# Performance work log

Hardware: AMD Instinct MI355X
Metric: run time of the kernel (lower is better)

Reference implementation:

```python
import jax, jax.numpy as jnp
import numpy as np

# Model dims (match init_kwargs)
D_MODEL = 2048
N_HEADS = 16
N_GROUPS = 8
HEAD_DIM = 128
TPA_RANK = 2
TPA_Q_RANK = 6


def setup_inputs() -> dict:
    key = jax.random.key(0)
    ks = jax.random.split(key, 7)
    S, B = 4096, 2
    scale = 1.0 / np.sqrt(D_MODEL)
    inp = {
        "hidden_states": jax.random.normal(ks[0], (S, B, D_MODEL), jnp.float32),
        # weights stored [in, out] so projection is x @ W
        "W_a_q": jax.random.normal(ks[1], (D_MODEL, N_HEADS * TPA_Q_RANK), jnp.float32) * scale,
        "W_a_k": jax.random.normal(ks[2], (D_MODEL, N_GROUPS * TPA_RANK), jnp.float32) * scale,
        "W_a_v": jax.random.normal(ks[3], (D_MODEL, N_GROUPS * TPA_RANK), jnp.float32) * scale,
        "W_b_q": jax.random.normal(ks[4], (D_MODEL, TPA_Q_RANK * HEAD_DIM), jnp.float32) * scale,
        "W_b_k": jax.random.normal(ks[5], (D_MODEL, TPA_RANK * HEAD_DIM), jnp.float32) * scale,
        "W_b_v": jax.random.normal(ks[6], (D_MODEL, TPA_RANK * HEAD_DIM), jnp.float32) * scale,
    }
    return inp


def reference(hidden_states, W_a_q, W_a_k, W_a_v, W_b_q, W_b_k, W_b_v):
    S, B, _ = hidden_states.shape
    x = hidden_states
    # Six column-parallel projections (world_size=1 -> full outputs)
    a_q = (x @ W_a_q).reshape(S, B, N_HEADS, TPA_Q_RANK)
    a_k = (x @ W_a_k).reshape(S, B, N_GROUPS, TPA_RANK)
    a_v = (x @ W_a_v).reshape(S, B, N_GROUPS, TPA_RANK)
    b_q = (x @ W_b_q).reshape(S, B, TPA_Q_RANK, HEAD_DIM)
    b_k = (x @ W_b_k).reshape(S, B, TPA_RANK, HEAD_DIM)
    b_v = (x @ W_b_v).reshape(S, B, TPA_RANK, HEAD_DIM)
    # Low-rank reconstruction: per-token batched matmul over the tiny rank dim
    q = jnp.einsum('sbhr,sbrd->sbhd', a_q, b_q) / TPA_Q_RANK  # [S,B,H,D]
    k = jnp.einsum('sbgr,sbrd->sbgd', a_k, b_k) / TPA_RANK    # [S,B,G,D]
    v = jnp.einsum('sbgr,sbrd->sbgd', a_v, b_v) / TPA_RANK    # [S,B,G,D]
    heads_per_group = N_HEADS // N_GROUPS
    q = q.reshape(S, B, N_GROUPS, heads_per_group * HEAD_DIM)
    mixed_qkv = jnp.concatenate([q, k, v], axis=3).reshape(S, B, -1)
    return mixed_qkv
```

## Files before the change

kernel.cpp:

```cpp
#include <hip/hip_runtime.h>
#include <hip/hip_bf16.h>

typedef __bf16 bf16x8 __attribute__((ext_vector_type(8)));
typedef float  f32x4  __attribute__((ext_vector_type(4)));

#define GLOAD_LDS16(g, l) \
  __builtin_amdgcn_global_load_lds((const __attribute__((address_space(1))) void*)(g), \
                                   (__attribute__((address_space(3))) void*)(l), 16, 0, 0)

static __device__ __forceinline__ ushort f2bf(float f) {
  union { float f; unsigned u; } x; x.f = f;
  unsigned r = x.u + 0x7fffu + ((x.u >> 16) & 1u);
  return (ushort)(r >> 16);
}
static __device__ __forceinline__ float bf2f(ushort u) {
  union { unsigned u; float f; } x; x.u = ((unsigned)u) << 16;
  return x.f;
}

__global__ void cast_x_k(const float4* __restrict__ in, ushort4* __restrict__ out, int n4) {
  int idx = blockIdx.x * 256 + threadIdx.x;
  int stride = gridDim.x * 256;
  for (int i = idx; i < n4; i += stride) {
    float4 v = in[i];
    ushort4 o;
    o.x = f2bf(v.x); o.y = f2bf(v.y); o.z = f2bf(v.z); o.w = f2bf(v.w);
    out[i] = o;
  }
}

__global__ void pack_wt_k(const float* __restrict__ W0, const float* __restrict__ W1,
                          const float* __restrict__ W2, const float* __restrict__ W3,
                          const float* __restrict__ W4, const float* __restrict__ W5,
                          ushort* __restrict__ Wt) {
  __shared__ ushort tile[64 * 66];
  const int k0 = blockIdx.x * 64, c0 = blockIdx.y * 64;
  const int tid = threadIdx.x;
#pragma unroll
  for (int i = 0; i < 16; ++i) {
    int idx = tid + i * 256;
    int kl = idx >> 6, cl = idx & 63;
    int c = c0 + cl, k = k0 + kl;
    const float* W; int n, lc;
    if (c < 96)       { W = W0; n = 96;  lc = c; }
    else if (c < 112) { W = W1; n = 16;  lc = c - 96; }
    else if (c < 128) { W = W2; n = 16;  lc = c - 112; }
    else if (c < 896) { W = W3; n = 768; lc = c - 128; }
    else if (c < 1152){ W = W4; n = 256; lc = c - 896; }
    else              { W = W5; n = 256; lc = c - 1152; }
    tile[cl * 66 + kl] = f2bf(W[(size_t)k * n + lc]);
  }
  __syncthreads();
#pragma unroll
  for (int i = 0; i < 16; ++i) {
    int idx = tid + i * 256;
    int cl = idx >> 6, kl = idx & 63;
    Wt[(size_t)(c0 + cl) * 2048 + (k0 + kl)] = tile[cl * 66 + kl];
  }
}

__global__ __launch_bounds__(256) void gemm_bt_k(const ushort* __restrict__ X,
                                                 const ushort* __restrict__ Wt,
                                                 ushort* __restrict__ Y) {
  __shared__ ushort lds[2][8192];
  const int tid = threadIdx.x;
  const int w = tid >> 6, lane = tid & 63;
  const int bid = blockIdx.x;
  const int wg = (bid & 7) * 88 + (bid >> 3);
  const int bm = wg & 63, bn = wg >> 6;
  const int wr = w >> 1, wc = w & 1;

  const int s0 = w, s1 = w + 4;
  const int ra = s0 * 16 + (lane >> 2);
  const int rb = s1 * 16 + (lane >> 2);
  const int ga = (lane & 3) ^ ((ra >> 1) & 3);
  const int gb = (lane & 3) ^ ((rb >> 1) & 3);
  const ushort* gA0 = X  + (size_t)(bm * 128 + ra) * 2048 + ga * 8;
  const ushort* gA1 = X  + (size_t)(bm * 128 + rb) * 2048 + gb * 8;
  const ushort* gB0 = Wt + (size_t)(bn * 128 + ra) * 2048 + ga * 8;
  const ushort* gB1 = Wt + (size_t)(bn * 128 + rb) * 2048 + gb * 8;
  const int lo0 = s0 * 512, lo1 = s1 * 512;

  int offA[4], offB[4];
#pragma unroll
  for (int m = 0; m < 4; ++m) {
    int R = wr * 64 + m * 16 + (lane & 15);
    offA[m] = R * 32 + ((((lane >> 4) ^ ((R >> 1) & 3))) << 3);
    int C = wc * 64 + m * 16 + (lane & 15);
    offB[m] = 4096 + C * 32 + ((((lane >> 4) ^ ((C >> 1) & 3))) << 3);
  }

  GLOAD_LDS16(gA0, &lds[0][lo0]);
  GLOAD_LDS16(gA1, &lds[0][lo1]);
  GLOAD_LDS16(gB0, &lds[0][4096 + lo0]);
  GLOAD_LDS16(gB1, &lds[0][4096 + lo1]);
  __syncthreads();

  f32x4 acc[4][4] = {};
  int cur = 0;

  for (int kk = 0; kk < 64; ++kk) {
    if (kk < 63) {
      const int ko = (kk + 1) * 32;
      ushort* nb = lds[cur ^ 1];
      GLOAD_LDS16(gA0 + ko, nb + lo0);
      GLOAD_LDS16(gA1 + ko, nb + lo1);
      GLOAD_LDS16(gB0 + ko, nb + 4096 + lo0);
      GLOAD_LDS16(gB1 + ko, nb + 4096 + lo1);
    }
    const ushort* cb = lds[cur];
    bf16x8 a[4], b[4];
#pragma unroll
    for (int m = 0; m < 4; ++m) a[m] = *reinterpret_cast<const bf16x8*>(&cb[offA[m]]);
#pragma unroll
    for (int n = 0; n < 4; ++n) b[n] = *reinterpret_cast<const bf16x8*>(&cb[offB[n]]);
#pragma unroll
    for (int m = 0; m < 4; ++m)
#pragma unroll
      for (int n = 0; n < 4; ++n)
        acc[m][n] = __builtin_amdgcn_mfma_f32_16x16x32_bf16(a[m], b[n], acc[m][n], 0, 0, 0);

    __syncthreads();
    cur ^= 1;
  }

#pragma unroll
  for (int m = 0; m < 4; ++m) {
    int row0 = bm * 128 + wr * 64 + m * 16 + ((lane >> 4) << 2);
#pragma unroll
    for (int n = 0; n < 4; ++n) {
      int col = bn * 128 + wc * 64 + n * 16 + (lane & 15);
#pragma unroll
      for (int j = 0; j < 4; ++j)
        Y[(size_t)(row0 + j) * 1408 + col] = f2bf(acc[m][n][j]);
    }
  }
}

__global__ void recon_k(const ushort* __restrict__ Y, float4* __restrict__ out) {
  __shared__ float L[1408];
  const int t = blockIdx.x, tid = threadIdx.x;
  const ushort* src = Y + (size_t)t * 1408;
  if (tid < 176) {
    ushort4 v0 = ((const ushort4*)src)[tid * 2];
    ushort4 v1 = ((const ushort4*)src)[tid * 2 + 1];
    float* d = L + tid * 8;
    d[0] = bf2f(v0.x); d[1] = bf2f(v0.y); d[2] = bf2f(v0.z); d[3] = bf2f(v0.w);
    d[4] = bf2f(v1.x); d[5] = bf2f(v1.y); d[6] = bf2f(v1.z); d[7] = bf2f(v1.w);
  }
  __syncthreads();
  float4* o = out + (size_t)t * 1024;
#pragma unroll
  for (int i = 0; i < 4; ++i) {
    int q4 = tid + (i << 8);
    int p = q4 << 2;
    int g = p >> 9, sub = p & 511;
    float4 val;
    if (sub < 256) {
      int h = (g << 1) + (sub >> 7), d = sub & 127;
      const float* a = L + h * 6;
      const float* b = L + 128 + d;
#pragma unroll
      for (int c = 0; c < 4; ++c)
        (&val.x)[c] = (a[0] * b[c] + a[1] * b[128 + c] + a[2] * b[256 + c] +
                       a[3] * b[384 + c] + a[4] * b[512 + c] + a[5] * b[640 + c]) * (1.0f / 6.0f);
    } else if (sub < 384) {
      int d = sub - 256;
      float a0 = L[96 + (g << 1)], a1 = L[97 + (g << 1)];
#pragma unroll
      for (int c = 0; c < 4; ++c)
        (&val.x)[c] = 0.5f * (a0 * L[896 + d + c] + a1 * L[1024 + d + c]);
    } else {
      int d = sub - 384;
      float a0 = L[112 + (g << 1)], a1 = L[113 + (g << 1)];
#pragma unroll
      for (int c = 0; c < 4; ++c)
        (&val.x)[c] = 0.5f * (a0 * L[1152 + d + c] + a1 * L[1280 + d + c]);
    }
    o[q4] = val;
  }
}

extern "C" void kernel_launch(void* const* d_in, const int* in_sizes, int n_in,
                              void* d_out, int out_size, void* d_ws, size_t ws_size,
                              hipStream_t stream) {
  const float* x   = (const float*)d_in[0];
  const float* Waq = (const float*)d_in[1];
  const float* Wak = (const float*)d_in[2];
  const float* Wav = (const float*)d_in[3];
  const float* Wbq = (const float*)d_in[4];
  const float* Wbk = (const float*)d_in[5];
  const float* Wbv = (const float*)d_in[6];

  ushort* Xbf = (ushort*)d_ws;
  ushort* Wt  = (ushort*)((char*)d_ws + 33554432);
  ushort* Y   = (ushort*)((char*)d_ws + 39321600);
  float*  out = (float*)d_out;

  cast_x_k<<<2048, 256, 0, stream>>>((const float4*)x, (ushort4*)Xbf, 16777216 / 4);
  pack_wt_k<<<dim3(32, 22), 256, 0, stream>>>(Waq, Wak, Wav, Wbq, Wbk, Wbv, Wt);
  gemm_bt_k<<<704, 256, 0, stream>>>(Xbf, Wt, Y);
  recon_k<<<8192, 256, 0, stream>>>(Y, (float4*)out);
}
```

Before: 274.2 us.

## Triple-buffer GEMM LDS with explicit vmcnt waits and barriers

The GEMM main loop goes from double buffering to a three-stage LDS ring. Each stage is prefetched two steps ahead, and a partial s_waitcnt vmcnt lets the loop wait only for the oldest stage instead of doing a full __syncthreads drain. This is meant to hide global-to-LDS load latency behind MFMA work. LDS use grows from 32KB to 48KB per block, which may lower occupancy. The hand-written waitcnt and barrier sequence is fragile if the compiler emits other memory ops.

```diff
diff --git a/kernel.cpp b/kernel.cpp
--- a/kernel.cpp
+++ b/kernel.cpp
@@ -62,7 +62,7 @@
 __global__ __launch_bounds__(256) void gemm_bt_k(const ushort* __restrict__ X,
                                                  const ushort* __restrict__ Wt,
                                                  ushort* __restrict__ Y) {
-  __shared__ ushort lds[2][8192];
+  __shared__ ushort lds[3 * 8192];
   const int tid = threadIdx.x;
   const int w = tid >> 6, lane = tid & 63;
   const int bid = blockIdx.x;
@@ -90,39 +90,70 @@
     offB[m] = 4096 + C * 32 + ((((lane >> 4) ^ ((C >> 1) & 3))) << 3);
   }
 
-  GLOAD_LDS16(gA0, &lds[0][lo0]);
-  GLOAD_LDS16(gA1, &lds[0][lo1]);
-  GLOAD_LDS16(gB0, &lds[0][4096 + lo0]);
-  GLOAD_LDS16(gB1, &lds[0][4096 + lo1]);
-  __syncthreads();
-
   f32x4 acc[4][4] = {};
-  int cur = 0;
-
-  for (int kk = 0; kk < 64; ++kk) {
-    if (kk < 63) {
-      const int ko = (kk + 1) * 32;
-      ushort* nb = lds[cur ^ 1];
-      GLOAD_LDS16(gA0 + ko, nb + lo0);
-      GLOAD_LDS16(gA1 + ko, nb + lo1);
-      GLOAD_LDS16(gB0 + ko, nb + 4096 + lo0);
-      GLOAD_LDS16(gB1 + ko, nb + 4096 + lo1);
-    }
-    const ushort* cb = lds[cur];
-    bf16x8 a[4], b[4];
-#pragma unroll
-    for (int m = 0; m < 4; ++m) a[m] = *reinterpret_cast<const bf16x8*>(&cb[offA[m]]);
-#pragma unroll
-    for (int n = 0; n < 4; ++n) b[n] = *reinterpret_cast<const bf16x8*>(&cb[offB[n]]);
-#pragma unroll
-    for (int m = 0; m < 4; ++m)
-#pragma unroll
-      for (int n = 0; n < 4; ++n)
-        acc[m][n] = __builtin_amdgcn_mfma_f32_16x16x32_bf16(a[m], b[n], acc[m][n], 0, 0, 0);
-
-    __syncthreads();
-    cur ^= 1;
-  }
+
+#define STAGE(bufi, kstep) do { \
+    ushort* nb = &lds[(bufi) * 8192]; \
+    const int _ko = (kstep) * 32; \
+    GLOAD_LDS16(gA0 + _ko, nb + lo0); \
+    GLOAD_LDS16(gA1 + _ko, nb + lo1); \
+    GLOAD_LDS16(gB0 + _ko, nb + 4096 + lo0); \
+    GLOAD_LDS16(gB1 + _ko, nb + 4096 + lo1); \
+  } while (0)
+
+#define COMPUTE(bufi) do { \
+    const ushort* cb = &lds[(bufi) * 8192]; \
+    bf16x8 a[4], b[4]; \
+    _Pragma("unroll") \
+    for (int m = 0; m < 4; ++m) a[m] = *reinterpret_cast<const bf16x8*>(&cb[offA[m]]); \
+    _Pragma("unroll") \
+    for (int n = 0; n < 4; ++n) b[n] = *reinterpret_cast<const bf16x8*>(&cb[offB[n]]); \
+    _Pragma("unroll") \
+    for (int m = 0; m < 4; ++m) \
+      _Pragma("unroll") \
+      for (int n = 0; n < 4; ++n) \
+        acc[m][n] = __builtin_amdgcn_mfma_f32_16x16x32_bf16(a[m], b[n], acc[m][n], 0, 0, 0); \
+  } while (0)
+
+#define WAITV(n) asm volatile("s_waitcnt vmcnt(" #n ")" ::: "memory")
+#define WAITL()  asm volatile("s_waitcnt lgkmcnt(0)" ::: "memory")
+#define BAR()    __builtin_amdgcn_s_barrier()
+
+  STAGE(0, 0); STAGE(1, 1); STAGE(2, 2);
+
+#pragma unroll 1
+  for (int t = 0; t < 60; t += 3) {
+    WAITV(8); BAR();
+    COMPUTE(0);
+    WAITL(); BAR();
+    STAGE(0, t + 3);
+
+    WAITV(8); BAR();
+    COMPUTE(1);
+    WAITL(); BAR();
+    STAGE(1, t + 4);
+
+    WAITV(8); BAR();
+    COMPUTE(2);
+    WAITL(); BAR();
+    STAGE(2, t + 5);
+  }
+  WAITV(8); BAR();
+  COMPUTE(0);
+  WAITL(); BAR();
+  STAGE(0, 63);
+  WAITV(8); BAR();
+  COMPUTE(1);
+  WAITV(4); BAR();
+  COMPUTE(2);
+  WAITV(0); BAR();
+  COMPUTE(0);
+
+#undef STAGE
+#undef COMPUTE
+#undef WAITV
+#undef WAITL
+#undef BAR
 
 #pragma unroll
   for (int m = 0; m < 4; ++m) {
```

Measured after the change: 271.7 us. No clear change (-0.9%).

## Use 256x256 GEMM tiles with 4-stage LDS pipeline and padded N

Applied to the files above, without the earlier changes.

The GEMM moves from 128x128 tiles with 256 threads and double buffering to 256x256 tiles with 512 threads, eight waves and a four-stage global-to-LDS pipeline using explicit vmcnt waits and barriers. A and B staging is interleaved with two halves of the MFMA work under raised priority. N is padded from 1408 to 1536 so the weight matrix tiles evenly, which means pack_wt writes zeros for the extra columns and Y gets a larger stride. The goal is more data reuse per tile and better hiding of memory latency. The cost is 9% wasted compute on padding, 128KB of dynamic LDS, and only 192 blocks for roughly 256 CUs, which may leave some CUs idle.

```diff
diff --git a/kernel.cpp b/kernel.cpp
--- a/kernel.cpp
+++ b/kernel.cpp
@@ -41,14 +41,15 @@
     int idx = tid + i * 256;
     int kl = idx >> 6, cl = idx & 63;
     int c = c0 + cl, k = k0 + kl;
-    const float* W; int n, lc;
-    if (c < 96)       { W = W0; n = 96;  lc = c; }
-    else if (c < 112) { W = W1; n = 16;  lc = c - 96; }
-    else if (c < 128) { W = W2; n = 16;  lc = c - 112; }
-    else if (c < 896) { W = W3; n = 768; lc = c - 128; }
-    else if (c < 1152){ W = W4; n = 256; lc = c - 896; }
-    else              { W = W5; n = 256; lc = c - 1152; }
-    tile[cl * 66 + kl] = f2bf(W[(size_t)k * n + lc]);
+    float v;
+    if (c < 96)        v = W0[(size_t)k * 96  + c];
+    else if (c < 112)  v = W1[(size_t)k * 16  + (c - 96)];
+    else if (c < 128)  v = W2[(size_t)k * 16  + (c - 112)];
+    else if (c < 896)  v = W3[(size_t)k * 768 + (c - 128)];
+    else if (c < 1152) v = W4[(size_t)k * 256 + (c - 896)];
+    else if (c < 1408) v = W5[(size_t)k * 256 + (c - 1152)];
+    else               v = 0.0f;
+    tile[cl * 66 + kl] = f2bf(v);
   }
   __syncthreads();
 #pragma unroll
@@ -59,80 +60,107 @@
   }
 }
 
-__global__ __launch_bounds__(256) void gemm_bt_k(const ushort* __restrict__ X,
-                                                 const ushort* __restrict__ Wt,
-                                                 ushort* __restrict__ Y) {
-  __shared__ ushort lds[2][8192];
+__global__ __launch_bounds__(512, 2) void gemm_bt_k(const ushort* __restrict__ X,
+                                                    const ushort* __restrict__ Wt,
+                                                    ushort* __restrict__ Y) {
+  extern __shared__ ushort lds[];
   const int tid = threadIdx.x;
-  const int w = tid >> 6, lane = tid & 63;
+  const int wid = tid >> 6, lane = tid & 63;
   const int bid = blockIdx.x;
-  const int wg = (bid & 7) * 88 + (bid >> 3);
-  const int bm = wg & 63, bn = wg >> 6;
-  const int wr = w >> 1, wc = w & 1;
-
-  const int s0 = w, s1 = w + 4;
-  const int ra = s0 * 16 + (lane >> 2);
-  const int rb = s1 * 16 + (lane >> 2);
-  const int ga = (lane & 3) ^ ((ra >> 1) & 3);
-  const int gb = (lane & 3) ^ ((rb >> 1) & 3);
-  const ushort* gA0 = X  + (size_t)(bm * 128 + ra) * 2048 + ga * 8;
-  const ushort* gA1 = X  + (size_t)(bm * 128 + rb) * 2048 + gb * 8;
-  const ushort* gB0 = Wt + (size_t)(bn * 128 + ra) * 2048 + ga * 8;
-  const ushort* gB1 = Wt + (size_t)(bn * 128 + rb) * 2048 + gb * 8;
-  const int lo0 = s0 * 512, lo1 = s1 * 512;
-
-  int offA[4], offB[4];
-#pragma unroll
-  for (int m = 0; m < 4; ++m) {
-    int R = wr * 64 + m * 16 + (lane & 15);
-    offA[m] = R * 32 + ((((lane >> 4) ^ ((R >> 1) & 3))) << 3);
-    int C = wc * 64 + m * 16 + (lane & 15);
-    offB[m] = 4096 + C * 32 + ((((lane >> 4) ^ ((C >> 1) & 3))) << 3);
-  }
-
-  GLOAD_LDS16(gA0, &lds[0][lo0]);
-  GLOAD_LDS16(gA1, &lds[0][lo1]);
-  GLOAD_LDS16(gB0, &lds[0][4096 + lo0]);
-  GLOAD_LDS16(gB1, &lds[0][4096 + lo1]);
-  __syncthreads();
-
-  f32x4 acc[4][4] = {};
-  int cur = 0;
-
-  for (int kk = 0; kk < 64; ++kk) {
-    if (kk < 63) {
-      const int ko = (kk + 1) * 32;
-      ushort* nb = lds[cur ^ 1];
-      GLOAD_LDS16(gA0 + ko, nb + lo0);
-      GLOAD_LDS16(gA1 + ko, nb + lo1);
-      GLOAD_LDS16(gB0 + ko, nb + 4096 + lo0);
-      GLOAD_LDS16(gB1 + ko, nb + 4096 + lo1);
-    }
-    const ushort* cb = lds[cur];
-    bf16x8 a[4], b[4];
-#pragma unroll
-    for (int m = 0; m < 4; ++m) a[m] = *reinterpret_cast<const bf16x8*>(&cb[offA[m]]);
-#pragma unroll
-    for (int n = 0; n < 4; ++n) b[n] = *reinterpret_cast<const bf16x8*>(&cb[offB[n]]);
-#pragma unroll
-    for (int m = 0; m < 4; ++m)
-#pragma unroll
-      for (int n = 0; n < 4; ++n)
-        acc[m][n] = __builtin_amdgcn_mfma_f32_16x16x32_bf16(a[m], b[n], acc[m][n], 0, 0, 0);
-
-    __syncthreads();
-    cur ^= 1;
-  }
-
-#pragma unroll
-  for (int m = 0; m < 4; ++m) {
-    int row0 = bm * 128 + wr * 64 + m * 16 + ((lane >> 4) << 2);
+  const int wg = (bid & 7) * 24 + (bid >> 3);
+  const int bm = wg & 31, bn = wg >> 5;
+  const int wr = wid >> 2, wc = wid & 3;
+
+  const int srow0 = wid * 16 + (lane >> 2);
+  const int srow1 = 128 + srow0;
+  const int g0 = (lane & 3) ^ ((srow0 >> 1) & 3);
+  const int g1 = (lane & 3) ^ ((srow1 >> 1) & 3);
+  const ushort* gA0 = X  + (size_t)(bm * 256 + srow0) * 2048 + g0 * 8;
+  const ushort* gA1 = X  + (size_t)(bm * 256 + srow1) * 2048 + g1 * 8;
+  const ushort* gB0 = Wt + (size_t)(bn * 256 + srow0) * 2048 + g0 * 8;
+  const ushort* gB1 = Wt + (size_t)(bn * 256 + srow1) * 2048 + g1 * 8;
+  const int sA0 = wid * 1024, sA1 = 8192 + wid * 1024;
+  const int sB0 = 16384 + wid * 1024, sB1 = 24576 + wid * 1024;
+
+  int offA[8], offB[4];
+#pragma unroll
+  for (int m = 0; m < 8; ++m) {
+    int ra = wr * 128 + m * 16 + (lane & 15);
+    int s = (lane >> 4) ^ ((ra >> 1) & 3);
+    offA[m] = ra * 32 + s * 8;
+  }
+#pragma unroll
+  for (int n = 0; n < 4; ++n) {
+    int cb = wc * 64 + n * 16 + (lane & 15);
+    int s = (lane >> 4) ^ ((cb >> 1) & 3);
+    offB[n] = 8192 + cb * 32 + s * 8;
+  }
+
+#define STAGEA(bi, kt) do { char* _s = (char*)lds + (bi) * 32768; const int _ko = (kt) * 32; \
+    GLOAD_LDS16(gA0 + _ko, _s + sA0); GLOAD_LDS16(gA1 + _ko, _s + sA1); } while (0)
+#define STAGEB(bi, kt) do { char* _s = (char*)lds + (bi) * 32768; const int _ko = (kt) * 32; \
+    GLOAD_LDS16(gB0 + _ko, _s + sB0); GLOAD_LDS16(gB1 + _ko, _s + sB1); } while (0)
+#define FRAG(base, off) (*reinterpret_cast<const bf16x8*>((base) + (off)))
+#define BARM() asm volatile("s_barrier" ::: "memory")
+#define MF(mi, av) { \
+    acc[mi][0] = __builtin_amdgcn_mfma_f32_16x16x32_bf16(av, bq0, acc[mi][0], 0, 0, 0); \
+    acc[mi][1] = __builtin_amdgcn_mfma_f32_16x16x32_bf16(av, bq1, acc[mi][1], 0, 0, 0); \
+    acc[mi][2] = __builtin_amdgcn_mfma_f32_16x16x32_bf16(av, bq2, acc[mi][2], 0, 0, 0); \
+    acc[mi][3] = __builtin_amdgcn_mfma_f32_16x16x32_bf16(av, bq3, acc[mi][3], 0, 0, 0); }
+
+  f32x4 acc[8][4] = {};
+
+  STAGEA(0, 0); STAGEB(0, 0);
+  STAGEA(1, 1); STAGEB(1, 1);
+  STAGEA(2, 2); STAGEB(2, 2);
+
+#pragma unroll 1
+  for (int t = 0; t < 64; ++t) {
+    const ushort* cbuf = lds + (t & 3) * 16384;
+    const int nb = (t + 3) & 3;
+    if (t <= 61)      asm volatile("s_waitcnt vmcnt(8)" ::: "memory");
+    else if (t == 62) asm volatile("s_waitcnt vmcnt(4)" ::: "memory");
+    else              asm volatile("s_waitcnt vmcnt(0)" ::: "memory");
+    BARM();
+
+    bf16x8 af0 = FRAG(cbuf, offA[0]), af1 = FRAG(cbuf, offA[1]),
+           af2 = FRAG(cbuf, offA[2]), af3 = FRAG(cbuf, offA[3]);
+    bf16x8 bq0 = FRAG(cbuf, offB[0]), bq1 = FRAG(cbuf, offB[1]),
+           bq2 = FRAG(cbuf, offB[2]), bq3 = FRAG(cbuf, offB[3]);
+    if (t <= 60) STAGEA(nb, t + 3);
+    BARM();
+    __builtin_amdgcn_sched_barrier(0);
+    __builtin_amdgcn_s_setprio(1);
+    MF(0, af0) MF(1, af1) MF(2, af2) MF(3, af3)
+    __builtin_amdgcn_s_setprio(0);
+    BARM();
+
+    af0 = FRAG(cbuf, offA[4]); af1 = FRAG(cbuf, offA[5]);
+    af2 = FRAG(cbuf, offA[6]); af3 = FRAG(cbuf, offA[7]);
+    if (t <= 60) STAGEB(nb, t + 3);
+    BARM();
+    __builtin_amdgcn_sched_barrier(0);
+    __builtin_amdgcn_s_setprio(1);
+    MF(4, af0) MF(5, af1) MF(6, af2) MF(7, af3)
+    __builtin_amdgcn_s_setprio(0);
+    BARM();
+  }
+
+#undef STAGEA
+#undef STAGEB
+#undef FRAG
+#undef BARM
+#undef MF
+
+#pragma unroll
+  for (int m = 0; m < 8; ++m) {
+    int row0 = bm * 256 + wr * 128 + m * 16 + ((lane >> 4) << 2);
 #pragma unroll
     for (int n = 0; n < 4; ++n) {
-      int col = bn * 128 + wc * 64 + n * 16 + (lane & 15);
+      int col = bn * 256 + wc * 64 + n * 16 + (lane & 15);
 #pragma unroll
       for (int j = 0; j < 4; ++j)
-        Y[(size_t)(row0 + j) * 1408 + col] = f2bf(acc[m][n][j]);
+        Y[(size_t)(row0 + j) * 1536 + col] = f2bf(acc[m][n][j]);
     }
   }
 }
@@ -140,7 +168,7 @@
 __global__ void recon_k(const ushort* __restrict__ Y, float4* __restrict__ out) {
   __shared__ float L[1408];
   const int t = blockIdx.x, tid = threadIdx.x;
-  const ushort* src = Y + (size_t)t * 1408;
+  const ushort* src = Y + (size_t)t * 1536;
   if (tid < 176) {
     ushort4 v0 = ((const ushort4*)src)[tid * 2];
     ushort4 v1 = ((const ushort4*)src)[tid * 2 + 1];
@@ -194,11 +222,14 @@
 
   ushort* Xbf = (ushort*)d_ws;
   ushort* Wt  = (ushort*)((char*)d_ws + 33554432);
-  ushort* Y   = (ushort*)((char*)d_ws + 39321600);
+  ushort* Y   = (ushort*)((char*)d_ws + 39845888);
   float*  out = (float*)d_out;
 
+  hipFuncSetAttribute(reinterpret_cast<const void*>(gemm_bt_k),
+                      hipFuncAttributeMaxDynamicSharedMemorySize, 131072);
+
   cast_x_k<<<2048, 256, 0, stream>>>((const float4*)x, (ushort4*)Xbf, 16777216 / 4);
-  pack_wt_k<<<dim3(32, 22), 256, 0, stream>>>(Waq, Wak, Wav, Wbq, Wbk, Wbv, Wt);
-  gemm_bt_k<<<704, 256, 0, stream>>>(Xbf, Wt, Y);
+  pack_wt_k<<<dim3(32, 24), 256, 0, stream>>>(Waq, Wak, Wav, Wbq, Wbk, Wbv, Wt);
+  gemm_bt_k<<<192, 512, 131072, stream>>>(Xbf, Wt, Y);
   recon_k<<<8192, 256, 0, stream>>>(Y, (float4*)out);
 }
```

Result: slower. 287.8 us (+5.0%).
